# Optimization experiments

Hardware: AMD Instinct MI355X
Metric: run time of the kernel (lower is better)

The kernel has to match this reference:

```python
import jax, jax.numpy as jnp
import numpy as np

EPS = 1e-5  # torch GroupNorm default eps


def _pairwise_sqdist(x, y):
    # squared euclidean distance matrix, clamped at 0 for numerical safety
    d = (jnp.sum(x * x, -1)[:, None] + jnp.sum(y * y, -1)[None, :]
         - 2.0 * (x @ y.T))
    return jnp.maximum(d, 0.0)


def _pc_normalize(ref, src):
    # jointly center and scale both clouds to the unit sphere
    pts = jnp.concatenate([ref, src], axis=0)
    centroid = pts.mean(axis=0, keepdims=True)
    pts = pts - centroid
    m = jnp.max(jnp.linalg.norm(pts, axis=1))
    pts = pts / m
    n_ref = ref.shape[0]
    return pts[:n_ref], pts[n_ref:]


def _group_norm(x, gamma, beta, groups):
    N, C = x.shape
    xg = x.reshape(N, groups, C // groups)
    mean = xg.mean(-1, keepdims=True)
    var = jnp.mean((xg - mean) ** 2, -1, keepdims=True)
    xn = ((xg - mean) / jnp.sqrt(var + EPS)).reshape(N, C)
    return xn * gamma + beta


def setup_inputs() -> dict:
    key = jax.random.key(0)
    ks = jax.random.split(key, 8)
    N_ref, N_src, D = 128, 128, 256
    points_c = jax.random.normal(ks[0], (N_ref + N_src, 3), jnp.float32)
    ref_feats = jax.random.normal(ks[1], (N_ref, D), jnp.float32)
    src_feats = jax.random.normal(ks[2], (N_src, D), jnp.float32)
    # normalized features, as the '_norm' names suggest
    ref_feats = ref_feats / jnp.linalg.norm(ref_feats, axis=-1, keepdims=True)
    src_feats = src_feats / jnp.linalg.norm(src_feats, axis=-1, keepdims=True)
    # a valid rigid transform: random rotation + small translation
    A = jax.random.normal(ks[3], (3, 3), jnp.float32)
    Q, _ = jnp.linalg.qr(A)
    trans = jnp.eye(4, dtype=jnp.float32)
    trans = trans.at[:3, :3].set(Q)
    trans = trans.at[:3, 3].set(jax.random.normal(ks[4], (3,), jnp.float32) * 0.1)
    s = 1.0 / np.sqrt(512)
    return {
        'points_c': points_c,
        'ref_feats_c_norm': ref_feats,
        'src_feats_c_norm': src_feats,
        'trans': trans,
        'W1': jax.random.normal(ks[5], (256, 512), jnp.float32) * s,
        'b1': jnp.zeros((256,), jnp.float32),
        'g1': jnp.ones((256,), jnp.float32),
        'bt1': jnp.zeros((256,), jnp.float32),
        'W2': jax.random.normal(ks[6], (128, 256), jnp.float32) * (1.0 / np.sqrt(256)),
        'b2': jnp.zeros((128,), jnp.float32),
        'g2': jnp.ones((128,), jnp.float32),
        'bt2': jnp.zeros((128,), jnp.float32),
        'W3': jax.random.normal(ks[7], (2, 128), jnp.float32) * (1.0 / np.sqrt(128)),
        'b3': jnp.zeros((2,), jnp.float32),
        'ref_length': 128,
    }


def reference(points_c, ref_feats_c_norm, src_feats_c_norm, trans,
              W1, b1, g1, bt1, W2, b2, g2, bt2, W3, b3, ref_length):
    GROUPS = 8
    ref_points = points_c[:ref_length]
    src_points = points_c[ref_length:]
    # apply rigid transform to src points
    src_points = src_points @ trans[:3, :3].T + trans[:3, 3]
    ref_n, src_n = _pc_normalize(ref_points, src_points)

    dist_mat = jnp.exp(-_pairwise_sqdist(ref_n, src_n))  # [Nr, Ns]
    match_idx_ref = jnp.argmax(dist_mat, axis=1)
    match_idx_src = jnp.argmax(dist_mat, axis=0)
    min_dist_ref = jnp.max(dist_mat, axis=1)
    min_dist_src = jnp.max(dist_mat, axis=0)

    feat_score_mat = ref_feats_c_norm @ src_feats_c_norm.T  # [Nr, Ns]
    feat_match_idx_ref = jnp.argmax(feat_score_mat, axis=1)
    feat_match_idx_src = jnp.argmax(feat_score_mat, axis=0)
    feat_match_ref = jnp.max(feat_score_mat, axis=1)
    feat_match_src = jnp.max(feat_score_mat, axis=0)

    r_idx = jnp.arange(feat_score_mat.shape[0])
    c_idx = jnp.arange(feat_score_mat.shape[1])
    feat_score_ref = feat_score_mat[r_idx, match_idx_ref]
    feat_score_src = feat_score_mat[match_idx_src, c_idx]
    dist_ref = dist_mat[r_idx, feat_match_idx_ref]
    dist_src = dist_mat[feat_match_idx_src, c_idx]

    min_dist = jnp.concatenate([min_dist_ref, min_dist_src])
    feat_score = jnp.concatenate([feat_score_ref, feat_score_src])
    perm_d = jnp.argsort(-min_dist)  # descending sort
    d_m = min_dist[perm_d] * feat_score[perm_d]

    match_feat = jnp.concatenate([feat_match_ref, feat_match_src])
    match_dist = jnp.concatenate([dist_ref, dist_src])
    perm_f = jnp.argsort(-match_feat)
    m_d = match_dist[perm_f] * match_feat[perm_f]

    geo_out = jnp.concatenate([d_m, m_d])[None, :]  # [1, 512]

    h = _group_norm(geo_out @ W1.T + b1, g1, bt1, GROUPS)
    h = jax.nn.relu(h)
    h = _group_norm(h @ W2.T + b2, g2, bt2, GROUPS)
    h = jax.nn.relu(h)
    return h @ W3.T + b3  # [1, num_classes]
```

## Files before the change

### kernel.cpp

```cpp
#include <hip/hip_runtime.h>
#include <math.h>

#define NREF 128
#define NSRC 128
#define DIM  256
#define EPS  1e-5f

__global__ __launch_bounds__(512) void side_kernel(
    const float* __restrict__ points_c,
    const float* __restrict__ trans,
    const float* __restrict__ ref_feats,
    const float* __restrict__ src_feats,
    float* __restrict__ arrs)
{
    __shared__ float px[256], py[256], pz[256], nsq[256];
    __shared__ float wred[12];
    __shared__ float red[4];
    __shared__ float featLds[128];
    __shared__ float cvD[8]; __shared__ int ciD[8];
    __shared__ float cvF[8]; __shared__ int ciF[8];

    const int b = blockIdx.x;
    const int t = threadIdx.x;
    const int w = t >> 6, l = t & 63;

    const bool isRow = (b < NREF);
    const int  me    = isRow ? b : (b - NREF);

    float x = 0.f, y = 0.f, z = 0.f;
    if (t < 256) {
        x = points_c[3 * t + 0];
        y = points_c[3 * t + 1];
        z = points_c[3 * t + 2];
        if (t >= NREF) {
            float nx = trans[0] * x + trans[1] * y + trans[2]  * z + trans[3];
            float ny = trans[4] * x + trans[5] * y + trans[6]  * z + trans[7];
            float nz = trans[8] * x + trans[9] * y + trans[10] * z + trans[11];
            x = nx; y = ny; z = nz;
        }
    }

    const float* __restrict__ myrow = (isRow ? ref_feats : src_feats) + me * DIM;
    const float4* __restrict__ other = (const float4*)(isRow ? src_feats : ref_feats);
    const float4 r = ((const float4*)myrow)[l];

    float bfv = -2.f; int bfi = 0;
    for (int m = 0; m < 16; m += 2) {
        const int j0 = w * 16 + m, j1 = j0 + 1;
        const float4 a0 = other[j0 * 64 + l];
        const float4 a1 = other[j1 * 64 + l];
        float acc0 = a0.x * r.x + a0.y * r.y + a0.z * r.z + a0.w * r.w;
        float acc1 = a1.x * r.x + a1.y * r.y + a1.z * r.z + a1.w * r.w;
        for (int off = 32; off >= 1; off >>= 1) {
            acc0 += __shfl_xor(acc0, off);
            acc1 += __shfl_xor(acc1, off);
        }
        if (l == 0) { featLds[j0] = acc0; featLds[j1] = acc1; }
        if (acc0 > bfv) { bfv = acc0; bfi = j0; }
        if (acc1 > bfv) { bfv = acc1; bfi = j1; }
    }
    if (l == 0) { cvF[w] = bfv; ciF[w] = bfi; }

    if (t < 256) {
        float sx = x, sy = y, sz = z;
        for (int off = 32; off >= 1; off >>= 1) {
            sx += __shfl_down(sx, off);
            sy += __shfl_down(sy, off);
            sz += __shfl_down(sz, off);
        }
        if (l == 0) { wred[w] = sx; wred[4 + w] = sy; wred[8 + w] = sz; }
    }
    __syncthreads();
    if (t == 0) {
        red[0] = (wred[0] + wred[1] + wred[2] + wred[3]) * (1.0f / 256.0f);
        red[1] = (wred[4] + wred[5] + wred[6] + wred[7]) * (1.0f / 256.0f);
        red[2] = (wred[8] + wred[9] + wred[10] + wred[11]) * (1.0f / 256.0f);
    }
    __syncthreads();
    if (t < 256) {
        x -= red[0]; y -= red[1]; z -= red[2];
        float n = x * x + y * y + z * z;
        float mx = n;
        for (int off = 32; off >= 1; off >>= 1)
            mx = fmaxf(mx, __shfl_down(mx, off));
        if (l == 0) wred[w] = mx;
    }
    __syncthreads();
    if (t == 0)
        red[3] = 1.0f / sqrtf(fmaxf(fmaxf(wred[0], wred[1]), fmaxf(wred[2], wred[3])));
    __syncthreads();
    if (t < 256) {
        const float inv = red[3];
        x *= inv; y *= inv; z *= inv;
        px[t] = x; py[t] = y; pz[t] = z;
        nsq[t] = x * x + y * y + z * z;
    }
    __syncthreads();

    float bdv = -1.f; int bdi = 0;
    for (int m = 0; m < 16; ++m) {
        const int jj = w * 16 + m;
        const int i = isRow ? me : jj;
        const int j = isRow ? jj : me;
        float d = nsq[i] + nsq[128 + j]
                - 2.0f * (px[i] * px[128 + j] + py[i] * py[128 + j] + pz[i] * pz[128 + j]);
        d = fmaxf(d, 0.f);
        const float v = expf(-d);
        if (v > bdv) { bdv = v; bdi = jj; }
    }
    if (l == 0) { cvD[w] = bdv; ciD[w] = bdi; }
    __syncthreads();

    if (t == 0) {
        float bv = -1.f; int bi = 0;
        for (int q = 0; q < 8; ++q)
            if (cvD[q] > bv) { bv = cvD[q]; bi = ciD[q]; }
        float fv = -2.f; int fi = 0;
        for (int q = 0; q < 8; ++q)
            if (cvF[q] > fv) { fv = cvF[q]; fi = ciF[q]; }
        const float fscore = featLds[bi];
        const int i = isRow ? me : fi;
        const int j = isRow ? fi : me;
        float d = nsq[i] + nsq[128 + j]
                - 2.0f * (px[i] * px[128 + j] + py[i] * py[128 + j] + pz[i] * pz[128 + j]);
        d = fmaxf(d, 0.f);
        const float mdist = expf(-d);
        const int gi = isRow ? me : NREF + me;
        arrs[gi]       = bv;
        arrs[256 + gi] = fscore;
        arrs[512 + gi] = fv;
        arrs[768 + gi] = mdist;
    }
}

__global__ __launch_bounds__(256) void mlp1_kernel(
    const float* __restrict__ arrs,
    const float* __restrict__ W1, const float* __restrict__ b1,
    float* __restrict__ y1)
{
    __shared__ __align__(16) float arrD[256], arrFS[256], arrMF[256], arrMD[256];
    __shared__ __align__(16) float geoLds[512];
    const int c = blockIdx.x;
    const int t = threadIdx.x;

    arrD[t]  = arrs[t];
    arrFS[t] = arrs[256 + t];
    arrMF[t] = arrs[512 + t];
    arrMD[t] = arrs[768 + t];
    __syncthreads();

    {
        const float vD = arrD[t];
        const float vF = arrMF[t];
        int rD = 0, rF = 0;
        for (int jb = 0; jb < 64; ++jb) {
            const float4 uD = ((const float4*)arrD)[jb];
            const float4 uF = ((const float4*)arrMF)[jb];
            const int j0 = 4 * jb;
            rD += (uD.x > vD) || (uD.x == vD && (j0 + 0) < t);
            rD += (uD.y > vD) || (uD.y == vD && (j0 + 1) < t);
            rD += (uD.z > vD) || (uD.z == vD && (j0 + 2) < t);
            rD += (uD.w > vD) || (uD.w == vD && (j0 + 3) < t);
            rF += (uF.x > vF) || (uF.x == vF && (j0 + 0) < t);
            rF += (uF.y > vF) || (uF.y == vF && (j0 + 1) < t);
            rF += (uF.z > vF) || (uF.z == vF && (j0 + 2) < t);
            rF += (uF.w > vF) || (uF.w == vF && (j0 + 3) < t);
        }
        geoLds[rD]       = vD * arrFS[t];
        geoLds[256 + rF] = arrMD[t] * vF;
    }
    __syncthreads();

    if (t < 64) {
        const int l = t;
        const float4 ga = ((const float4*)geoLds)[l];
        const float4 gb = ((const float4*)geoLds)[64 + l];
        const float4* __restrict__ wrow = (const float4*)(W1 + c * 512);
        const float4 a = wrow[l];
        const float4 b = wrow[64 + l];
        float acc = a.x * ga.x + a.y * ga.y + a.z * ga.z + a.w * ga.w
                  + b.x * gb.x + b.y * gb.y + b.z * gb.z + b.w * gb.w;
        acc += __shfl_down(acc, 32);
        acc += __shfl_down(acc, 16);
        acc += __shfl_down(acc, 8);
        acc += __shfl_down(acc, 4);
        acc += __shfl_down(acc, 2);
        acc += __shfl_down(acc, 1);
        if (l == 0) y1[c] = acc + b1[c];
    }
}

__global__ __launch_bounds__(64) void mlp2_kernel(
    const float* __restrict__ y1,
    const float* __restrict__ g1, const float* __restrict__ bt1,
    const float* __restrict__ W2, const float* __restrict__ b2,
    float* __restrict__ y2)
{
    __shared__ __align__(16) float y1s[256];
    __shared__ float stats[16];
    const int c = blockIdx.x, l = threadIdx.x;
    ((float4*)y1s)[l] = ((const float4*)y1)[l];
    __syncthreads();
    if (l < 8) {
        float s = 0.f;
        for (int k = 0; k < 32; ++k) s += y1s[(l << 5) + k];
        const float mean = s * (1.0f / 32.0f);
        float q = 0.f;
        for (int k = 0; k < 32; ++k) { const float d = y1s[(l << 5) + k] - mean; q += d * d; }
        const float var = q * (1.0f / 32.0f);
        stats[l] = mean;
        stats[8 + l] = rsqrtf(var + EPS);
    }
    __syncthreads();
    const float4 gg = ((const float4*)g1)[l];
    const float4 bb = ((const float4*)bt1)[l];
    const int g = l >> 3;
    const float mean = stats[g], inv = stats[8 + g];
    const float4 yv = ((const float4*)y1s)[l];
    float4 h;
    h.x = fmaxf((yv.x - mean) * inv * gg.x + bb.x, 0.f);
    h.y = fmaxf((yv.y - mean) * inv * gg.y + bb.y, 0.f);
    h.z = fmaxf((yv.z - mean) * inv * gg.z + bb.z, 0.f);
    h.w = fmaxf((yv.w - mean) * inv * gg.w + bb.w, 0.f);
    const float4 wv = ((const float4*)(W2 + c * 256))[l];
    float acc = wv.x * h.x + wv.y * h.y + wv.z * h.z + wv.w * h.w;
    acc += __shfl_down(acc, 32);
    acc += __shfl_down(acc, 16);
    acc += __shfl_down(acc, 8);
    acc += __shfl_down(acc, 4);
    acc += __shfl_down(acc, 2);
    acc += __shfl_down(acc, 1);
    if (l == 0) y2[c] = acc + b2[c];
}

__global__ __launch_bounds__(128) void final_kernel(
    const float* __restrict__ y2,
    const float* __restrict__ g2, const float* __restrict__ bt2,
    const float* __restrict__ W3, const float* __restrict__ b3,
    float* __restrict__ out)
{
    __shared__ float y2s[128], h2[128];
    const int t = threadIdx.x;
    y2s[t] = y2[t];
    __syncthreads();
    {
        const int g = t >> 4;
        float s = 0.f;
        for (int k = 0; k < 16; ++k) s += y2s[(g << 4) + k];
        const float mean = s * (1.0f / 16.0f);
        float q = 0.f;
        for (int k = 0; k < 16; ++k) { const float d = y2s[(g << 4) + k] - mean; q += d * d; }
        const float var = q * (1.0f / 16.0f);
        const float xn = (y2s[t] - mean) * rsqrtf(var + EPS);
        h2[t] = fmaxf(xn * g2[t] + bt2[t], 0.f);
    }
    __syncthreads();
    const int wave = t >> 6, lane = t & 63;
    float acc = W3[wave * 128 + lane] * h2[lane]
              + W3[wave * 128 + 64 + lane] * h2[64 + lane];
    acc += __shfl_down(acc, 32);
    acc += __shfl_down(acc, 16);
    acc += __shfl_down(acc, 8);
    acc += __shfl_down(acc, 4);
    acc += __shfl_down(acc, 2);
    acc += __shfl_down(acc, 1);
    if (lane == 0) out[wave] = acc + b3[wave];
}

extern "C" void kernel_launch(void* const* d_in, const int* in_sizes, int n_in,
                              void* d_out, int out_size, void* d_ws, size_t ws_size,
                              hipStream_t stream)
{
    const float* points_c  = (const float*)d_in[0];
    const float* ref_feats = (const float*)d_in[1];
    const float* src_feats = (const float*)d_in[2];
    const float* trans     = (const float*)d_in[3];
    const float* W1  = (const float*)d_in[4];
    const float* b1  = (const float*)d_in[5];
    const float* g1  = (const float*)d_in[6];
    const float* bt1 = (const float*)d_in[7];
    const float* W2  = (const float*)d_in[8];
    const float* b2  = (const float*)d_in[9];
    const float* g2  = (const float*)d_in[10];
    const float* bt2 = (const float*)d_in[11];
    const float* W3  = (const float*)d_in[12];
    const float* b3  = (const float*)d_in[13];

    float* arrs = (float*)d_ws;
    float* y1   = arrs + 1024;
    float* y2   = arrs + 1280;

    side_kernel<<<dim3(256), dim3(512), 0, stream>>>(points_c, trans, ref_feats, src_feats, arrs);
    mlp1_kernel<<<dim3(256), dim3(256), 0, stream>>>(arrs, W1, b1, y1);
    mlp2_kernel<<<dim3(128), dim3(64), 0, stream>>>(y1, g1, bt1, W2, b2, y2);
    final_kernel<<<dim3(1), dim3(128), 0, stream>>>(y2, g2, bt2, W3, b3, (float*)d_out);
}
```

Before: 104.3 us.

## Fuse four kernels into one cooperative kernel with grid syncs

Merges the side, mlp1, mlp2 and final kernels into one cooperative kernel launched with 256 blocks of 512 threads. Grid-wide syncs with thread fences replace the kernel boundaries between stages. This removes three kernel launches and their inter-kernel gaps. In exchange it pays grid.sync cost three times, needs all 256 blocks co-resident, and uses more shared memory per block, which may lower occupancy.

New measurement: 387.9 us. 272% more time.

```diff
diff --git a/kernel.cpp b/kernel.cpp
--- a/kernel.cpp
+++ b/kernel.cpp
@@ -1,270 +1,284 @@
 #include <hip/hip_runtime.h>
+#include <hip/hip_cooperative_groups.h>
 #include <math.h>
+
+namespace cg = cooperative_groups;
 
 #define NREF 128
 #define NSRC 128
 #define DIM  256
 #define EPS  1e-5f
 
-__global__ __launch_bounds__(512) void side_kernel(
+__global__ __launch_bounds__(512) void fused_kernel(
     const float* __restrict__ points_c,
     const float* __restrict__ trans,
     const float* __restrict__ ref_feats,
     const float* __restrict__ src_feats,
-    float* __restrict__ arrs)
+    const float* __restrict__ W1, const float* __restrict__ b1,
+    const float* __restrict__ g1, const float* __restrict__ bt1,
+    const float* __restrict__ W2, const float* __restrict__ b2,
+    const float* __restrict__ g2, const float* __restrict__ bt2,
+    const float* __restrict__ W3, const float* __restrict__ b3,
+    float* __restrict__ arrs,
+    float* __restrict__ out)
 {
+    cg::grid_group grid = cg::this_grid();
+
     __shared__ float px[256], py[256], pz[256], nsq[256];
     __shared__ float wred[12];
     __shared__ float red[4];
     __shared__ float featLds[128];
     __shared__ float cvD[8]; __shared__ int ciD[8];
     __shared__ float cvF[8]; __shared__ int ciF[8];
-
-    const int b = blockIdx.x;
+    __shared__ __align__(16) float arrD[256], arrFS[256], arrMF[256], arrMD[256];
+    __shared__ __align__(16) float geoLds[512];
+    __shared__ __align__(16) float y1s[256];
+    __shared__ float stats[16];
+    __shared__ float y2s[128], h2s[128];
+
+    float* __restrict__ y1g = arrs + 1024;
+    float* __restrict__ y2g = arrs + 1280;
+
     const int t = threadIdx.x;
     const int w = t >> 6, l = t & 63;
 
-    const bool isRow = (b < NREF);
-    const int  me    = isRow ? b : (b - NREF);
-
-    float x = 0.f, y = 0.f, z = 0.f;
-    if (t < 256) {
-        x = points_c[3 * t + 0];
-        y = points_c[3 * t + 1];
-        z = points_c[3 * t + 2];
-        if (t >= NREF) {
-            float nx = trans[0] * x + trans[1] * y + trans[2]  * z + trans[3];
-            float ny = trans[4] * x + trans[5] * y + trans[6]  * z + trans[7];
-            float nz = trans[8] * x + trans[9] * y + trans[10] * z + trans[11];
-            x = nx; y = ny; z = nz;
+    {
+        const int b = blockIdx.x;
+        const bool isRow = (b < NREF);
+        const int  me    = isRow ? b : (b - NREF);
+
+        float x = 0.f, y = 0.f, z = 0.f;
+        if (t < 256) {
+            x = points_c[3 * t + 0];
+            y = points_c[3 * t + 1];
+            z = points_c[3 * t + 2];
+            if (t >= NREF) {
+                float nx = trans[0] * x + trans[1] * y + trans[2]  * z + trans[3];
+                float ny = trans[4] * x + trans[5] * y + trans[6]  * z + trans[7];
+                float nz = trans[8] * x + trans[9] * y + trans[10] * z + trans[11];
+                x = nx; y = ny; z = nz;
+            }
+        }
+
+        const float* __restrict__ myrow = (isRow ? ref_feats : src_feats) + me * DIM;
+        const float4* __restrict__ other = (const float4*)(isRow ? src_feats : ref_feats);
+        const float4 r = ((const float4*)myrow)[l];
+
+        float bfv = -2.f; int bfi = 0;
+        for (int m = 0; m < 16; m += 2) {
+            const int j0 = w * 16 + m, j1 = j0 + 1;
+            const float4 a0 = other[j0 * 64 + l];
+            const float4 a1 = other[j1 * 64 + l];
+            float acc0 = a0.x * r.x + a0.y * r.y + a0.z * r.z + a0.w * r.w;
+            float acc1 = a1.x * r.x + a1.y * r.y + a1.z * r.z + a1.w * r.w;
+            for (int off = 32; off >= 1; off >>= 1) {
+                acc0 += __shfl_xor(acc0, off);
+                acc1 += __shfl_xor(acc1, off);
+            }
+            if (l == 0) { featLds[j0] = acc0; featLds[j1] = acc1; }
+            if (acc0 > bfv) { bfv = acc0; bfi = j0; }
+            if (acc1 > bfv) { bfv = acc1; bfi = j1; }
+        }
+        if (l == 0) { cvF[w] = bfv; ciF[w] = bfi; }
+
+        if (t < 256) {
+            float sx = x, sy = y, sz = z;
+            for (int off = 32; off >= 1; off >>= 1) {
+                sx += __shfl_down(sx, off);
+                sy += __shfl_down(sy, off);
+                sz += __shfl_down(sz, off);
+            }
+            if (l == 0) { wred[w] = sx; wred[4 + w] = sy; wred[8 + w] = sz; }
+        }
+        __syncthreads();
+        if (t == 0) {
+            red[0] = (wred[0] + wred[1] + wred[2] + wred[3]) * (1.0f / 256.0f);
+            red[1] = (wred[4] + wred[5] + wred[6] + wred[7]) * (1.0f / 256.0f);
+            red[2] = (wred[8] + wred[9] + wred[10] + wred[11]) * (1.0f / 256.0f);
+        }
+        __syncthreads();
+        if (t < 256) {
+            x -= red[0]; y -= red[1]; z -= red[2];
+            float n = x * x + y * y + z * z;
+            float mx = n;
+            for (int off = 32; off >= 1; off >>= 1)
+                mx = fmaxf(mx, __shfl_down(mx, off));
+            if (l == 0) wred[w] = mx;
+        }
+        __syncthreads();
+        if (t == 0)
+            red[3] = 1.0f / sqrtf(fmaxf(fmaxf(wred[0], wred[1]), fmaxf(wred[2], wred[3])));
+        __syncthreads();
+        if (t < 256) {
+            const float inv = red[3];
+            x *= inv; y *= inv; z *= inv;
+            px[t] = x; py[t] = y; pz[t] = z;
+            nsq[t] = x * x + y * y + z * z;
+        }
+        __syncthreads();
+
+        float bdv = -1.f; int bdi = 0;
+        for (int m = 0; m < 16; ++m) {
+            const int jj = w * 16 + m;
+            const int i = isRow ? me : jj;
+            const int j = isRow ? jj : me;
+            float d = nsq[i] + nsq[128 + j]
+                    - 2.0f * (px[i] * px[128 + j] + py[i] * py[128 + j] + pz[i] * pz[128 + j]);
+            d = fmaxf(d, 0.f);
+            const float v = expf(-d);
+            if (v > bdv) { bdv = v; bdi = jj; }
+        }
+        if (l == 0) { cvD[w] = bdv; ciD[w] = bdi; }
+        __syncthreads();
+
+        if (t == 0) {
+            float bv = -1.f; int bi = 0;
+            for (int q = 0; q < 8; ++q)
+                if (cvD[q] > bv) { bv = cvD[q]; bi = ciD[q]; }
+            float fv = -2.f; int fi = 0;
+            for (int q = 0; q < 8; ++q)
+                if (cvF[q] > fv) { fv = cvF[q]; fi = ciF[q]; }
+            const float fscore = featLds[bi];
+            const int i = isRow ? me : fi;
+            const int j = isRow ? fi : me;
+            float d = nsq[i] + nsq[128 + j]
+                    - 2.0f * (px[i] * px[128 + j] + py[i] * py[128 + j] + pz[i] * pz[128 + j]);
+            d = fmaxf(d, 0.f);
+            const float mdist = expf(-d);
+            const int gi = isRow ? me : NREF + me;
+            arrs[gi]       = bv;
+            arrs[256 + gi] = fscore;
+            arrs[512 + gi] = fv;
+            arrs[768 + gi] = mdist;
         }
     }
 
-    const float* __restrict__ myrow = (isRow ? ref_feats : src_feats) + me * DIM;
-    const float4* __restrict__ other = (const float4*)(isRow ? src_feats : ref_feats);
-    const float4 r = ((const float4*)myrow)[l];
-
-    float bfv = -2.f; int bfi = 0;
-    for (int m = 0; m < 16; m += 2) {
-        const int j0 = w * 16 + m, j1 = j0 + 1;
-        const float4 a0 = other[j0 * 64 + l];
-        const float4 a1 = other[j1 * 64 + l];
-        float acc0 = a0.x * r.x + a0.y * r.y + a0.z * r.z + a0.w * r.w;
-        float acc1 = a1.x * r.x + a1.y * r.y + a1.z * r.z + a1.w * r.w;
-        for (int off = 32; off >= 1; off >>= 1) {
-            acc0 += __shfl_xor(acc0, off);
-            acc1 += __shfl_xor(acc1, off);
-        }
-        if (l == 0) { featLds[j0] = acc0; featLds[j1] = acc1; }
-        if (acc0 > bfv) { bfv = acc0; bfi = j0; }
-        if (acc1 > bfv) { bfv = acc1; bfi = j1; }
+    __threadfence();
+    grid.sync();
+    __threadfence();
+
+    {
+        const int c = blockIdx.x;
+        if (t < 256) {
+            arrD[t]  = arrs[t];
+            arrFS[t] = arrs[256 + t];
+            arrMF[t] = arrs[512 + t];
+            arrMD[t] = arrs[768 + t];
+        }
+        __syncthreads();
+        if (t < 256) {
+            const float vD = arrD[t];
+            const float vF = arrMF[t];
+            int rD = 0, rF = 0;
+            for (int jb = 0; jb < 64; ++jb) {
+                const float4 uD = ((const float4*)arrD)[jb];
+                const float4 uF = ((const float4*)arrMF)[jb];
+                const int j0 = 4 * jb;
+                rD += (uD.x > vD) || (uD.x == vD && (j0 + 0) < t);
+                rD += (uD.y > vD) || (uD.y == vD && (j0 + 1) < t);
+                rD += (uD.z > vD) || (uD.z == vD && (j0 + 2) < t);
+                rD += (uD.w > vD) || (uD.w == vD && (j0 + 3) < t);
+                rF += (uF.x > vF) || (uF.x == vF && (j0 + 0) < t);
+                rF += (uF.y > vF) || (uF.y == vF && (j0 + 1) < t);
+                rF += (uF.z > vF) || (uF.z == vF && (j0 + 2) < t);
+                rF += (uF.w > vF) || (uF.w == vF && (j0 + 3) < t);
+            }
+            geoLds[rD]       = vD * arrFS[t];
+            geoLds[256 + rF] = arrMD[t] * vF;
+        }
+        __syncthreads();
+        if (t < 64) {
+            const float4 ga = ((const float4*)geoLds)[t];
+            const float4 gb = ((const float4*)geoLds)[64 + t];
+            const float4* __restrict__ wrow = (const float4*)(W1 + c * 512);
+            const float4 a = wrow[t];
+            const float4 b = wrow[64 + t];
+            float acc = a.x * ga.x + a.y * ga.y + a.z * ga.z + a.w * ga.w
+                      + b.x * gb.x + b.y * gb.y + b.z * gb.z + b.w * gb.w;
+            acc += __shfl_down(acc, 32);
+            acc += __shfl_down(acc, 16);
+            acc += __shfl_down(acc, 8);
+            acc += __shfl_down(acc, 4);
+            acc += __shfl_down(acc, 2);
+            acc += __shfl_down(acc, 1);
+            if (t == 0) y1g[c] = acc + b1[c];
+        }
     }
-    if (l == 0) { cvF[w] = bfv; ciF[w] = bfi; }
-
-    if (t < 256) {
-        float sx = x, sy = y, sz = z;
-        for (int off = 32; off >= 1; off >>= 1) {
-            sx += __shfl_down(sx, off);
-            sy += __shfl_down(sy, off);
-            sz += __shfl_down(sz, off);
-        }
-        if (l == 0) { wred[w] = sx; wred[4 + w] = sy; wred[8 + w] = sz; }
+
+    __threadfence();
+    grid.sync();
+    __threadfence();
+
+    if (blockIdx.x < 128) {
+        const int c = blockIdx.x;
+        if (t < 64) ((float4*)y1s)[t] = ((const float4*)y1g)[t];
+        __syncthreads();
+        if (t < 8) {
+            float s = 0.f;
+            for (int k = 0; k < 32; ++k) s += y1s[(t << 5) + k];
+            const float mean = s * (1.0f / 32.0f);
+            float q = 0.f;
+            for (int k = 0; k < 32; ++k) { const float d = y1s[(t << 5) + k] - mean; q += d * d; }
+            const float var = q * (1.0f / 32.0f);
+            stats[t] = mean;
+            stats[8 + t] = rsqrtf(var + EPS);
+        }
+        __syncthreads();
+        if (t < 64) {
+            const float4 gg = ((const float4*)g1)[t];
+            const float4 bb = ((const float4*)bt1)[t];
+            const int g = t >> 3;
+            const float mean = stats[g], inv = stats[8 + g];
+            const float4 yv = ((const float4*)y1s)[t];
+            float4 h;
+            h.x = fmaxf((yv.x - mean) * inv * gg.x + bb.x, 0.f);
+            h.y = fmaxf((yv.y - mean) * inv * gg.y + bb.y, 0.f);
+            h.z = fmaxf((yv.z - mean) * inv * gg.z + bb.z, 0.f);
+            h.w = fmaxf((yv.w - mean) * inv * gg.w + bb.w, 0.f);
+            const float4 wv = ((const float4*)(W2 + c * 256))[t];
+            float acc = wv.x * h.x + wv.y * h.y + wv.z * h.z + wv.w * h.w;
+            acc += __shfl_down(acc, 32);
+            acc += __shfl_down(acc, 16);
+            acc += __shfl_down(acc, 8);
+            acc += __shfl_down(acc, 4);
+            acc += __shfl_down(acc, 2);
+            acc += __shfl_down(acc, 1);
+            if (t == 0) y2g[c] = acc + b2[c];
+        }
     }
-    __syncthreads();
-    if (t == 0) {
-        red[0] = (wred[0] + wred[1] + wred[2] + wred[3]) * (1.0f / 256.0f);
-        red[1] = (wred[4] + wred[5] + wred[6] + wred[7]) * (1.0f / 256.0f);
-        red[2] = (wred[8] + wred[9] + wred[10] + wred[11]) * (1.0f / 256.0f);
+
+    __threadfence();
+    grid.sync();
+    __threadfence();
+
+    if (blockIdx.x == 0) {
+        if (t < 128) y2s[t] = y2g[t];
+        __syncthreads();
+        if (t < 128) {
+            const int g = t >> 4;
+            float s = 0.f;
+            for (int k = 0; k < 16; ++k) s += y2s[(g << 4) + k];
+            const float mean = s * (1.0f / 16.0f);
+            float q = 0.f;
+            for (int k = 0; k < 16; ++k) { const float d = y2s[(g << 4) + k] - mean; q += d * d; }
+            const float var = q * (1.0f / 16.0f);
+            const float xn = (y2s[t] - mean) * rsqrtf(var + EPS);
+            h2s[t] = fmaxf(xn * g2[t] + bt2[t], 0.f);
+        }
+        __syncthreads();
+        if (t < 128) {
+            const int wave = t >> 6, lane = t & 63;
+            float acc = W3[wave * 128 + lane] * h2s[lane]
+                      + W3[wave * 128 + 64 + lane] * h2s[64 + lane];
+            acc += __shfl_down(acc, 32);
+            acc += __shfl_down(acc, 16);
+            acc += __shfl_down(acc, 8);
+            acc += __shfl_down(acc, 4);
+            acc += __shfl_down(acc, 2);
+            acc += __shfl_down(acc, 1);
+            if (lane == 0) out[wave] = acc + b3[wave];
+        }
     }
-    __syncthreads();
-    if (t < 256) {
-        x -= red[0]; y -= red[1]; z -= red[2];
-        float n = x * x + y * y + z * z;
-        float mx = n;
-        for (int off = 32; off >= 1; off >>= 1)
-            mx = fmaxf(mx, __shfl_down(mx, off));
-        if (l == 0) wred[w] = mx;
-    }
-    __syncthreads();
-    if (t == 0)
-        red[3] = 1.0f / sqrtf(fmaxf(fmaxf(wred[0], wred[1]), fmaxf(wred[2], wred[3])));
-    __syncthreads();
-    if (t < 256) {
-        const float inv = red[3];
-        x *= inv; y *= inv; z *= inv;
-        px[t] = x; py[t] = y; pz[t] = z;
-        nsq[t] = x * x + y * y + z * z;
-    }
-    __syncthreads();
-
-    float bdv = -1.f; int bdi = 0;
-    for (int m = 0; m < 16; ++m) {
-        const int jj = w * 16 + m;
-        const int i = isRow ? me : jj;
-        const int j = isRow ? jj : me;
-        float d = nsq[i] + nsq[128 + j]
-                - 2.0f * (px[i] * px[128 + j] + py[i] * py[128 + j] + pz[i] * pz[128 + j]);
-        d = fmaxf(d, 0.f);
-        const float v = expf(-d);
-        if (v > bdv) { bdv = v; bdi = jj; }
-    }
-    if (l == 0) { cvD[w] = bdv; ciD[w] = bdi; }
-    __syncthreads();
-
-    if (t == 0) {
-        float bv = -1.f; int bi = 0;
-        for (int q = 0; q < 8; ++q)
-            if (cvD[q] > bv) { bv = cvD[q]; bi = ciD[q]; }
-        float fv = -2.f; int fi = 0;
-        for (int q = 0; q < 8; ++q)
-            if (cvF[q] > fv) { fv = cvF[q]; fi = ciF[q]; }
-        const float fscore = featLds[bi];
-        const int i = isRow ? me : fi;
-        const int j = isRow ? fi : me;
-        float d = nsq[i] + nsq[128 + j]
-                - 2.0f * (px[i] * px[128 + j] + py[i] * py[128 + j] + pz[i] * pz[128 + j]);
-        d = fmaxf(d, 0.f);
-        const float mdist = expf(-d);
-        const int gi = isRow ? me : NREF + me;
-        arrs[gi]       = bv;
-        arrs[256 + gi] = fscore;
-        arrs[512 + gi] = fv;
-        arrs[768 + gi] = mdist;
-    }
-}
-
-__global__ __launch_bounds__(256) void mlp1_kernel(
-    const float* __restrict__ arrs,
-    const float* __restrict__ W1, const float* __restrict__ b1,
-    float* __restrict__ y1)
-{
-    __shared__ __align__(16) float arrD[256], arrFS[256], arrMF[256], arrMD[256];
-    __shared__ __align__(16) float geoLds[512];
-    const int c = blockIdx.x;
-    const int t = threadIdx.x;
-
-    arrD[t]  = arrs[t];
-    arrFS[t] = arrs[256 + t];
-    arrMF[t] = arrs[512 + t];
-    arrMD[t] = arrs[768 + t];
-    __syncthreads();
-
-    {
-        const float vD = arrD[t];
-        const float vF = arrMF[t];
-        int rD = 0, rF = 0;
-        for (int jb = 0; jb < 64; ++jb) {
-            const float4 uD = ((const float4*)arrD)[jb];
-            const float4 uF = ((const float4*)arrMF)[jb];
-            const int j0 = 4 * jb;
-            rD += (uD.x > vD) || (uD.x == vD && (j0 + 0) < t);
-            rD += (uD.y > vD) || (uD.y == vD && (j0 + 1) < t);
-            rD += (uD.z > vD) || (uD.z == vD && (j0 + 2) < t);
-            rD += (uD.w > vD) || (uD.w == vD && (j0 + 3) < t);
-            rF += (uF.x > vF) || (uF.x == vF && (j0 + 0) < t);
-            rF += (uF.y > vF) || (uF.y == vF && (j0 + 1) < t);
-            rF += (uF.z > vF) || (uF.z == vF && (j0 + 2) < t);
-            rF += (uF.w > vF) || (uF.w == vF && (j0 + 3) < t);
-        }
-        geoLds[rD]       = vD * arrFS[t];
-        geoLds[256 + rF] = arrMD[t] * vF;
-    }
-    __syncthreads();
-
-    if (t < 64) {
-        const int l = t;
-        const float4 ga = ((const float4*)geoLds)[l];
-        const float4 gb = ((const float4*)geoLds)[64 + l];
-        const float4* __restrict__ wrow = (const float4*)(W1 + c * 512);
-        const float4 a = wrow[l];
-        const float4 b = wrow[64 + l];
-        float acc = a.x * ga.x + a.y * ga.y + a.z * ga.z + a.w * ga.w
-                  + b.x * gb.x + b.y * gb.y + b.z * gb.z + b.w * gb.w;
-        acc += __shfl_down(acc, 32);
-        acc += __shfl_down(acc, 16);
-        acc += __shfl_down(acc, 8);
-        acc += __shfl_down(acc, 4);
-        acc += __shfl_down(acc, 2);
-        acc += __shfl_down(acc, 1);
-        if (l == 0) y1[c] = acc + b1[c];
-    }
-}
-
-__global__ __launch_bounds__(64) void mlp2_kernel(
-    const float* __restrict__ y1,
-    const float* __restrict__ g1, const float* __restrict__ bt1,
-    const float* __restrict__ W2, const float* __restrict__ b2,
-    float* __restrict__ y2)
-{
-    __shared__ __align__(16) float y1s[256];
-    __shared__ float stats[16];
-    const int c = blockIdx.x, l = threadIdx.x;
-    ((float4*)y1s)[l] = ((const float4*)y1)[l];
-    __syncthreads();
-    if (l < 8) {
-        float s = 0.f;
-        for (int k = 0; k < 32; ++k) s += y1s[(l << 5) + k];
-        const float mean = s * (1.0f / 32.0f);
-        float q = 0.f;
-        for (int k = 0; k < 32; ++k) { const float d = y1s[(l << 5) + k] - mean; q += d * d; }
-        const float var = q * (1.0f / 32.0f);
-        stats[l] = mean;
-        stats[8 + l] = rsqrtf(var + EPS);
-    }
-    __syncthreads();
-    const float4 gg = ((const float4*)g1)[l];
-    const float4 bb = ((const float4*)bt1)[l];
-    const int g = l >> 3;
-    const float mean = stats[g], inv = stats[8 + g];
-    const float4 yv = ((const float4*)y1s)[l];
-    float4 h;
-    h.x = fmaxf((yv.x - mean) * inv * gg.x + bb.x, 0.f);
-    h.y = fmaxf((yv.y - mean) * inv * gg.y + bb.y, 0.f);
-    h.z = fmaxf((yv.z - mean) * inv * gg.z + bb.z, 0.f);
-    h.w = fmaxf((yv.w - mean) * inv * gg.w + bb.w, 0.f);
-    const float4 wv = ((const float4*)(W2 + c * 256))[l];
-    float acc = wv.x * h.x + wv.y * h.y + wv.z * h.z + wv.w * h.w;
-    acc += __shfl_down(acc, 32);
-    acc += __shfl_down(acc, 16);
-    acc += __shfl_down(acc, 8);
-    acc += __shfl_down(acc, 4);
-    acc += __shfl_down(acc, 2);
-    acc += __shfl_down(acc, 1);
-    if (l == 0) y2[c] = acc + b2[c];
-}
-
-__global__ __launch_bounds__(128) void final_kernel(
-    const float* __restrict__ y2,
-    const float* __restrict__ g2, const float* __restrict__ bt2,
-    const float* __restrict__ W3, const float* __restrict__ b3,
-    float* __restrict__ out)
-{
-    __shared__ float y2s[128], h2[128];
-    const int t = threadIdx.x;
-    y2s[t] = y2[t];
-    __syncthreads();
-    {
-        const int g = t >> 4;
-        float s = 0.f;
-        for (int k = 0; k < 16; ++k) s += y2s[(g << 4) + k];
-        const float mean = s * (1.0f / 16.0f);
-        float q = 0.f;
-        for (int k = 0; k < 16; ++k) { const float d = y2s[(g << 4) + k] - mean; q += d * d; }
-        const float var = q * (1.0f / 16.0f);
-        const float xn = (y2s[t] - mean) * rsqrtf(var + EPS);
-        h2[t] = fmaxf(xn * g2[t] + bt2[t], 0.f);
-    }
-    __syncthreads();
-    const int wave = t >> 6, lane = t & 63;
-    float acc = W3[wave * 128 + lane] * h2[lane]
-              + W3[wave * 128 + 64 + lane] * h2[64 + lane];
-    acc += __shfl_down(acc, 32);
-    acc += __shfl_down(acc, 16);
-    acc += __shfl_down(acc, 8);
-    acc += __shfl_down(acc, 4);
-    acc += __shfl_down(acc, 2);
-    acc += __shfl_down(acc, 1);
-    if (lane == 0) out[wave] = acc + b3[wave];
 }
 
 extern "C" void kernel_launch(void* const* d_in, const int* in_sizes, int n_in,
@@ -287,11 +301,15 @@
     const float* b3  = (const float*)d_in[13];
 
     float* arrs = (float*)d_ws;
-    float* y1   = arrs + 1024;
-    float* y2   = arrs + 1280;
-
-    side_kernel<<<dim3(256), dim3(512), 0, stream>>>(points_c, trans, ref_feats, src_feats, arrs);
-    mlp1_kernel<<<dim3(256), dim3(256), 0, stream>>>(arrs, W1, b1, y1);
-    mlp2_kernel<<<dim3(128), dim3(64), 0, stream>>>(y1, g1, bt1, W2, b2, y2);
-    final_kernel<<<dim3(1), dim3(128), 0, stream>>>(y2, g2, bt2, W3, b3, (float*)d_out);
+    float* outp = (float*)d_out;
+
+    void* args[] = {
+        (void*)&points_c, (void*)&trans, (void*)&ref_feats, (void*)&src_feats,
+        (void*)&W1, (void*)&b1, (void*)&g1, (void*)&bt1,
+        (void*)&W2, (void*)&b2, (void*)&g2, (void*)&bt2,
+        (void*)&W3, (void*)&b3,
+        (void*)&arrs, (void*)&outp
+    };
+    hipLaunchCooperativeKernel((const void*)fused_kernel,
+                               dim3(256), dim3(512), args, 0, stream);
 }
```

## Fuse MLP tail into one kernel and prefetch later-stage weights into cache

Applied to the files above, without the earlier changes.

The mlp2 and final kernels are merged into a single 512-thread tail kernel, dropping one launch and the y2 round trip through global memory. Earlier kernels now issue dummy loads of W1, W2, W3 and the norm parameters so these weights sit in L2 before the kernels that use them run. The side kernel's feature loads are also hoisted into a register array to raise memory-level parallelism. The cost is that the tail now runs on a single block, serialising the W2 GEMV that previously used 128 blocks, and the register use of the unrolled arrays goes up.

Result: slower. 108.9 us (+4.4%).

```diff
diff --git a/kernel.cpp b/kernel.cpp
--- a/kernel.cpp
+++ b/kernel.cpp
@@ -11,6 +11,7 @@
     const float* __restrict__ trans,
     const float* __restrict__ ref_feats,
     const float* __restrict__ src_feats,
+    const float* __restrict__ W1,
     float* __restrict__ arrs)
 {
     __shared__ float px[256], py[256], pz[256], nsq[256];
@@ -26,6 +27,8 @@
 
     const bool isRow = (b < NREF);
     const int  me    = isRow ? b : (b - NREF);
+
+    const float4 w1warm = ((const float4*)(W1 + (size_t)b * 512))[t & 127];
 
     float x = 0.f, y = 0.f, z = 0.f;
     if (t < 256) {
@@ -44,13 +47,17 @@
     const float4* __restrict__ other = (const float4*)(isRow ? src_feats : ref_feats);
     const float4 r = ((const float4*)myrow)[l];
 
+    float4 av[16];
+    #pragma unroll
+    for (int m = 0; m < 16; ++m)
+        av[m] = other[(w * 16 + m) * 64 + l];
+
     float bfv = -2.f; int bfi = 0;
+    #pragma unroll
     for (int m = 0; m < 16; m += 2) {
         const int j0 = w * 16 + m, j1 = j0 + 1;
-        const float4 a0 = other[j0 * 64 + l];
-        const float4 a1 = other[j1 * 64 + l];
-        float acc0 = a0.x * r.x + a0.y * r.y + a0.z * r.z + a0.w * r.w;
-        float acc1 = a1.x * r.x + a1.y * r.y + a1.z * r.z + a1.w * r.w;
+        float acc0 = av[m].x * r.x + av[m].y * r.y + av[m].z * r.z + av[m].w * r.w;
+        float acc1 = av[m+1].x * r.x + av[m+1].y * r.y + av[m+1].z * r.z + av[m+1].w * r.w;
         for (int off = 32; off >= 1; off >>= 1) {
             acc0 += __shfl_xor(acc0, off);
             acc1 += __shfl_xor(acc1, off);
@@ -131,17 +138,41 @@
         arrs[512 + gi] = fv;
         arrs[768 + gi] = mdist;
     }
+
+    asm volatile("" :: "v"(w1warm.x), "v"(w1warm.y), "v"(w1warm.z), "v"(w1warm.w));
 }
 
 __global__ __launch_bounds__(256) void mlp1_kernel(
     const float* __restrict__ arrs,
     const float* __restrict__ W1, const float* __restrict__ b1,
+    const float* __restrict__ W2,
+    const float* __restrict__ g1, const float* __restrict__ bt1,
+    const float* __restrict__ W3, const float* __restrict__ b2,
+    const float* __restrict__ g2, const float* __restrict__ bt2,
     float* __restrict__ y1)
 {
     __shared__ __align__(16) float arrD[256], arrFS[256], arrMF[256], arrMD[256];
     __shared__ __align__(16) float geoLds[512];
     const int c = blockIdx.x;
     const int t = threadIdx.x;
+
+    float4 warm = make_float4(0.f, 0.f, 0.f, 0.f);
+    if (c < 128 && t < 64)
+        warm = ((const float4*)(W2 + (size_t)c * 256))[t];
+    else if (c == 128 && t < 64)
+        warm = ((const float4*)W3)[t];
+    else if (c == 129 && t < 64)
+        warm = ((const float4*)g1)[t];
+    else if (c == 130 && t < 64)
+        warm = ((const float4*)bt1)[t];
+    else if (c == 131 && t < 32)
+        warm = ((const float4*)g2)[t];
+    else if (c == 132 && t < 32)
+        warm = ((const float4*)bt2)[t];
+    else if (c == 133 && t < 32)
+        warm = ((const float4*)b2)[t];
+
+    const float b1c = b1[c];
 
     arrD[t]  = arrs[t];
     arrFS[t] = arrs[256 + t];
@@ -172,12 +203,11 @@
     __syncthreads();
 
     if (t < 64) {
-        const int l = t;
-        const float4 ga = ((const float4*)geoLds)[l];
-        const float4 gb = ((const float4*)geoLds)[64 + l];
+        const float4 ga = ((const float4*)geoLds)[t];
+        const float4 gb = ((const float4*)geoLds)[64 + t];
         const float4* __restrict__ wrow = (const float4*)(W1 + c * 512);
-        const float4 a = wrow[l];
-        const float4 b = wrow[64 + l];
+        const float4 a = wrow[t];
+        const float4 b = wrow[64 + t];
         float acc = a.x * ga.x + a.y * ga.y + a.z * ga.z + a.w * ga.w
                   + b.x * gb.x + b.y * gb.y + b.z * gb.z + b.w * gb.w;
         acc += __shfl_down(acc, 32);
@@ -186,64 +216,76 @@
         acc += __shfl_down(acc, 4);
         acc += __shfl_down(acc, 2);
         acc += __shfl_down(acc, 1);
-        if (l == 0) y1[c] = acc + b1[c];
-    }
+        if (t == 0) y1[c] = acc + b1c;
+    }
+
+    asm volatile("" :: "v"(warm.x), "v"(warm.y), "v"(warm.z), "v"(warm.w));
 }
 
-__global__ __launch_bounds__(64) void mlp2_kernel(
+__global__ __launch_bounds__(512) void tail_kernel(
     const float* __restrict__ y1,
     const float* __restrict__ g1, const float* __restrict__ bt1,
     const float* __restrict__ W2, const float* __restrict__ b2,
-    float* __restrict__ y2)
-{
-    __shared__ __align__(16) float y1s[256];
-    __shared__ float stats[16];
-    const int c = blockIdx.x, l = threadIdx.x;
-    ((float4*)y1s)[l] = ((const float4*)y1)[l];
-    __syncthreads();
-    if (l < 8) {
-        float s = 0.f;
-        for (int k = 0; k < 32; ++k) s += y1s[(l << 5) + k];
-        const float mean = s * (1.0f / 32.0f);
-        float q = 0.f;
-        for (int k = 0; k < 32; ++k) { const float d = y1s[(l << 5) + k] - mean; q += d * d; }
-        const float var = q * (1.0f / 32.0f);
-        stats[l] = mean;
-        stats[8 + l] = rsqrtf(var + EPS);
-    }
-    __syncthreads();
-    const float4 gg = ((const float4*)g1)[l];
-    const float4 bb = ((const float4*)bt1)[l];
-    const int g = l >> 3;
-    const float mean = stats[g], inv = stats[8 + g];
-    const float4 yv = ((const float4*)y1s)[l];
-    float4 h;
-    h.x = fmaxf((yv.x - mean) * inv * gg.x + bb.x, 0.f);
-    h.y = fmaxf((yv.y - mean) * inv * gg.y + bb.y, 0.f);
-    h.z = fmaxf((yv.z - mean) * inv * gg.z + bb.z, 0.f);
-    h.w = fmaxf((yv.w - mean) * inv * gg.w + bb.w, 0.f);
-    const float4 wv = ((const float4*)(W2 + c * 256))[l];
-    float acc = wv.x * h.x + wv.y * h.y + wv.z * h.z + wv.w * h.w;
-    acc += __shfl_down(acc, 32);
-    acc += __shfl_down(acc, 16);
-    acc += __shfl_down(acc, 8);
-    acc += __shfl_down(acc, 4);
-    acc += __shfl_down(acc, 2);
-    acc += __shfl_down(acc, 1);
-    if (l == 0) y2[c] = acc + b2[c];
-}
-
-__global__ __launch_bounds__(128) void final_kernel(
-    const float* __restrict__ y2,
     const float* __restrict__ g2, const float* __restrict__ bt2,
     const float* __restrict__ W3, const float* __restrict__ b3,
     float* __restrict__ out)
 {
-    __shared__ float y2s[128], h2[128];
+    __shared__ __align__(16) float y1s[256];
+    __shared__ float stats[16];
+    __shared__ __align__(16) float b2s[128];
+    __shared__ float y2s[128], h2s[128];
+
     const int t = threadIdx.x;
-    y2s[t] = y2[t];
-    __syncthreads();
+    const int w = t >> 6, l = t & 63;
+
+    float4 wv[16];
+    #pragma unroll
+    for (int m = 0; m < 16; ++m)
+        wv[m] = ((const float4*)(W2 + (size_t)(w * 16 + m) * 256))[l];
+
+    if (t < 64) ((float4*)y1s)[t] = ((const float4*)y1)[t];
+    if (t < 32) ((float4*)b2s)[t] = ((const float4*)b2)[t];
+    __syncthreads();
+
+    if (t < 8) {
+        float s = 0.f;
+        for (int k = 0; k < 32; ++k) s += y1s[(t << 5) + k];
+        const float mean = s * (1.0f / 32.0f);
+        float q = 0.f;
+        for (int k = 0; k < 32; ++k) { const float d = y1s[(t << 5) + k] - mean; q += d * d; }
+        const float var = q * (1.0f / 32.0f);
+        stats[t] = mean;
+        stats[8 + t] = rsqrtf(var + EPS);
+    }
+    __syncthreads();
+
     {
+        const float4 gg = ((const float4*)g1)[l];
+        const float4 bb = ((const float4*)bt1)[l];
+        const int g = l >> 3;
+        const float mean = stats[g], inv = stats[8 + g];
+        const float4 yv = ((const float4*)y1s)[l];
+        float4 h;
+        h.x = fmaxf((yv.x - mean) * inv * gg.x + bb.x, 0.f);
+        h.y = fmaxf((yv.y - mean) * inv * gg.y + bb.y, 0.f);
+        h.z = fmaxf((yv.z - mean) * inv * gg.z + bb.z, 0.f);
+        h.w = fmaxf((yv.w - mean) * inv * gg.w + bb.w, 0.f);
+
+        #pragma unroll
+        for (int m = 0; m < 16; ++m) {
+            float acc = wv[m].x * h.x + wv[m].y * h.y + wv[m].z * h.z + wv[m].w * h.w;
+            acc += __shfl_down(acc, 32);
+            acc += __shfl_down(acc, 16);
+            acc += __shfl_down(acc, 8);
+            acc += __shfl_down(acc, 4);
+            acc += __shfl_down(acc, 2);
+            acc += __shfl_down(acc, 1);
+            if (l == 0) y2s[w * 16 + m] = acc + b2s[w * 16 + m];
+        }
+    }
+    __syncthreads();
+
+    if (t < 128) {
         const int g = t >> 4;
         float s = 0.f;
         for (int k = 0; k < 16; ++k) s += y2s[(g << 4) + k];
@@ -252,19 +294,21 @@
         for (int k = 0; k < 16; ++k) { const float d = y2s[(g << 4) + k] - mean; q += d * d; }
         const float var = q * (1.0f / 16.0f);
         const float xn = (y2s[t] - mean) * rsqrtf(var + EPS);
-        h2[t] = fmaxf(xn * g2[t] + bt2[t], 0.f);
-    }
-    __syncthreads();
-    const int wave = t >> 6, lane = t & 63;
-    float acc = W3[wave * 128 + lane] * h2[lane]
-              + W3[wave * 128 + 64 + lane] * h2[64 + lane];
-    acc += __shfl_down(acc, 32);
-    acc += __shfl_down(acc, 16);
-    acc += __shfl_down(acc, 8);
-    acc += __shfl_down(acc, 4);
-    acc += __shfl_down(acc, 2);
-    acc += __shfl_down(acc, 1);
-    if (lane == 0) out[wave] = acc + b3[wave];
+        h2s[t] = fmaxf(xn * g2[t] + bt2[t], 0.f);
+    }
+    __syncthreads();
+    if (t < 128) {
+        const int wave = t >> 6, lane = t & 63;
+        float acc = W3[wave * 128 + lane] * h2s[lane]
+                  + W3[wave * 128 + 64 + lane] * h2s[64 + lane];
+        acc += __shfl_down(acc, 32);
+        acc += __shfl_down(acc, 16);
+        acc += __shfl_down(acc, 8);
+        acc += __shfl_down(acc, 4);
+        acc += __shfl_down(acc, 2);
+        acc += __shfl_down(acc, 1);
+        if (lane == 0) out[wave] = acc + b3[wave];
+    }
 }
 
 extern "C" void kernel_launch(void* const* d_in, const int* in_sizes, int n_in,
@@ -288,10 +332,11 @@
 
     float* arrs = (float*)d_ws;
     float* y1   = arrs + 1024;
-    float* y2   = arrs + 1280;
-
-    side_kernel<<<dim3(256), dim3(512), 0, stream>>>(points_c, trans, ref_feats, src_feats, arrs);
-    mlp1_kernel<<<dim3(256), dim3(256), 0, stream>>>(arrs, W1, b1, y1);
-    mlp2_kernel<<<dim3(128), dim3(64), 0, stream>>>(y1, g1, bt1, W2, b2, y2);
-    final_kernel<<<dim3(1), dim3(128), 0, stream>>>(y2, g2, bt2, W3, b3, (float*)d_out);
+
+    side_kernel<<<dim3(256), dim3(512), 0, stream>>>(points_c, trans, ref_feats,
+                                                     src_feats, W1, arrs);
+    mlp1_kernel<<<dim3(256), dim3(256), 0, stream>>>(arrs, W1, b1, W2,
+                                                     g1, bt1, W3, b2, g2, bt2, y1);
+    tail_kernel<<<dim3(1), dim3(512), 0, stream>>>(y1, g1, bt1, W2, b2,
+                                                   g2, bt2, W3, b3, (float*)d_out);
 }
```
